# Kernel optimization log

Hardware: AMD Instinct MI355X
Metric: run time of the kernel (lower is better)

Reference implementation:

```python
import jax, jax.numpy as jnp
import numpy as np

N_NODES = 50000
N_EDGES = 800000
IN_DIM = 128
HID = 8
HEADS = 8
OUT_DIM = 64
NEG_SLOPE = 0.2


def setup_inputs() -> dict:
    key = jax.random.key(0)
    ks = jax.random.split(key, 8)
    x = jax.random.normal(ks[0], (N_NODES, IN_DIM), dtype=jnp.float32)
    edge_index = jax.random.randint(ks[1], (2, N_EDGES), 0, N_NODES, dtype=jnp.int64)
    W1 = jax.random.normal(ks[2], (IN_DIM, HEADS * HID), dtype=jnp.float32) / np.sqrt(IN_DIM)
    a_src1 = jax.random.normal(ks[3], (HEADS, HID), dtype=jnp.float32)
    a_dst1 = jax.random.normal(ks[4], (HEADS, HID), dtype=jnp.float32)
    b1 = jnp.zeros((HEADS * HID,), dtype=jnp.float32)
    W2 = jax.random.normal(ks[5], (HEADS * HID, OUT_DIM), dtype=jnp.float32) / np.sqrt(HEADS * HID)
    a_src2 = jax.random.normal(ks[6], (1, OUT_DIM), dtype=jnp.float32)
    a_dst2 = jax.random.normal(ks[7], (1, OUT_DIM), dtype=jnp.float32)
    b2 = jnp.zeros((OUT_DIM,), dtype=jnp.float32)
    return {"x": x, "edge_index": edge_index, "W1": W1, "a_src1": a_src1,
            "a_dst1": a_dst1, "b1": b1, "W2": W2, "a_src2": a_src2,
            "a_dst2": a_dst2, "b2": b2}


def gat_conv(x, src, dst, W, a_src, a_dst, b, heads, ch):
    # PyG GATConv (eval mode): linear -> per-edge LeakyReLU score ->
    # segment-softmax over incoming edges -> weighted scatter-add -> +bias
    n = x.shape[0]
    h = (x @ W).reshape(n, heads, ch)               # [N,H,C]
    score_src = jnp.einsum('nhc,hc->nh', h, a_src)  # [N,H]
    score_dst = jnp.einsum('nhc,hc->nh', h, a_dst)  # [N,H]
    e = jax.nn.leaky_relu(score_src[src] + score_dst[dst], NEG_SLOPE)  # [E,H]
    m = jax.ops.segment_max(e, dst, num_segments=n)
    m = jnp.where(jnp.isfinite(m), m, 0.0)
    p = jnp.exp(e - m[dst])
    denom = jax.ops.segment_sum(p, dst, num_segments=n)
    alpha = p / (denom[dst] + 1e-16)                # [E,H]
    out = jax.ops.segment_sum(h[src] * alpha[:, :, None], dst, num_segments=n)
    return out.reshape(n, heads * ch) + b


def reference(x, edge_index, W1, a_src1, a_dst1, b1, W2, a_src2, a_dst2, b2):
    n = x.shape[0]
    # add_self_loops=True (PyG default)
    loops = jnp.arange(n, dtype=edge_index.dtype)
    src = jnp.concatenate([edge_index[0], loops])
    dst = jnp.concatenate([edge_index[1], loops])
    h = gat_conv(x, src, dst, W1, a_src1, a_dst1, b1, HEADS, HID)
    h = jax.nn.elu(h)
    out = gat_conv(h, src, dst, W2, a_src2, a_dst2, b2, 1, OUT_DIM)
    return out
```

## Files before the change

kernel.cpp:

```cpp
#include <hip/hip_runtime.h>
#include <hip/hip_fp16.h>
#include <math.h>
#include <stdint.h>

#define N_NODES 50000
#define N_EDGES 800000
#define ET (N_EDGES + N_NODES)
#define IN_DIM 128
#define H1DIM 64
#define HEADS 8
#define HID 8
#define OUT_DIM 64
#define NEG_SLOPE 0.2f

#define SCAN_TILE 256
#define NTILES ((N_NODES + SCAN_TILE - 1) / SCAN_TILE)
#define RC 8
#define PF 6

#define LIN1_WAVES (N_NODES / 16)
#define LIN1_BLOCKS ((LIN1_WAVES + 3) / 4)
#define LIN2_WAVES (N_NODES / 16)
#define LIN2_BLOCKS ((LIN2_WAVES + 3) / 4)
#define EB ((ET + 255) / 256)

typedef _Float16 half8 __attribute__((ext_vector_type(8)));
typedef float f32x4 __attribute__((ext_vector_type(4)));

__device__ __forceinline__ float lrelu(float v) { return v >= 0.f ? v : NEG_SLOPE * v; }

__device__ __forceinline__ int xcc_id() {
    int v;
    asm volatile("s_getreg_b32 %0, hwreg(HW_REG_XCC_ID)" : "=s"(v));
    return v & 7;
}

__device__ __forceinline__ void fma8raw(uint4 u, float alpha, float* a) {
    float2 f0 = __half22float2(*(const __half2*)&u.x);
    float2 f1 = __half22float2(*(const __half2*)&u.y);
    float2 f2 = __half22float2(*(const __half2*)&u.z);
    float2 f3 = __half22float2(*(const __half2*)&u.w);
    a[0] += f0.x * alpha; a[1] += f0.y * alpha;
    a[2] += f1.x * alpha; a[3] += f1.y * alpha;
    a[4] += f2.x * alpha; a[5] += f2.y * alpha;
    a[6] += f3.x * alpha; a[7] += f3.y * alpha;
}

__device__ __forceinline__ void fma8h(const __half* __restrict__ base, float alpha, float* a) {
    fma8raw(*reinterpret_cast<const uint4*>(base), alpha, a);
}

__device__ __forceinline__ void edge_nodes(const int* __restrict__ ei, int e, int& s, int& d) {
    if (e < N_EDGES) { s = ei[e]; d = ei[N_EDGES + e]; }
    else             { s = e - N_EDGES; d = s; }
}


__global__ __launch_bounds__(256) void cl1_kernel(
    const int* __restrict__ ei, int* __restrict__ cnt8, int* __restrict__ pos,
    const float* __restrict__ x, const float* __restrict__ W1,
    const float* __restrict__ a_src, const float* __restrict__ a_dst,
    __half* __restrict__ h1, float* __restrict__ ssrc, float* __restrict__ sdst)
{
    if (blockIdx.x >= LIN1_BLOCKS) {
        int i = (blockIdx.x - LIN1_BLOCKS) * 256 + threadIdx.x;
        if (i >= ET) return;
        int s, d; edge_nodes(ei, i, s, d);
        int c = xcc_id();
        int r = atomicAdd(&cnt8[c * N_NODES + d], 1);
        pos[i] = r | (c << 28);
        return;
    }

    __shared__ __half bH[16 * 512];
    __shared__ __half bL[16 * 512];

    int tid = threadIdx.x;
    #pragma unroll
    for (int i = 0; i < 32; ++i) {
        int idx = i * 256 + tid;
        int f = idx >> 9, rr = idx & 511;
        int l = rr >> 3, j = rr & 7;
        int ks = f >> 2, ct = f & 3;
        int k = ks * 32 + ((l >> 4) << 3) + j;
        int c = (ct << 4) + (l & 15);
        float w = W1[k * 64 + c];
        __half hi = __float2half(w);
        bH[idx] = hi;
        bL[idx] = __float2half(w - __half2float(hi));
    }
    __syncthreads();

    int wid = tid >> 6, t = tid & 63;
    int g = blockIdx.x * 4 + wid;
    if (g >= LIN1_WAVES) return;
    int n0 = g * 16;
    int row = t & 15, kq = t >> 4;

    f32x4 acc[4] = {};
    const float* xp = x + (size_t)(n0 + row) * IN_DIM + kq * 8;
    #pragma unroll
    for (int ks = 0; ks < 4; ++ks) {
        float4 u0 = *reinterpret_cast<const float4*>(xp + ks * 32);
        float4 u1 = *reinterpret_cast<const float4*>(xp + ks * 32 + 4);
        float xv[8] = {u0.x, u0.y, u0.z, u0.w, u1.x, u1.y, u1.z, u1.w};
        half8 ah, al;
        #pragma unroll
        for (int j = 0; j < 8; ++j) {
            _Float16 h = (_Float16)xv[j];
            ah[j] = h;
            al[j] = (_Float16)(xv[j] - (float)h);
        }
        #pragma unroll
        for (int ct = 0; ct < 4; ++ct) {
            int f = ks * 4 + ct;
            half8 bh = *reinterpret_cast<const half8*>(&bH[f * 512 + t * 8]);
            half8 bl = *reinterpret_cast<const half8*>(&bL[f * 512 + t * 8]);
            acc[ct] = __builtin_amdgcn_mfma_f32_16x16x32_f16(ah, bh, acc[ct], 0, 0, 0);
            acc[ct] = __builtin_amdgcn_mfma_f32_16x16x32_f16(al, bh, acc[ct], 0, 0, 0);
            acc[ct] = __builtin_amdgcn_mfma_f32_16x16x32_f16(ah, bl, acc[ct], 0, 0, 0);
        }
    }

    float asv[4], adv[4];
    #pragma unroll
    for (int ct = 0; ct < 4; ++ct) {
        asv[ct] = a_src[ct * 16 + (t & 15)];
        adv[ct] = a_dst[ct * 16 + (t & 15)];
    }
    int rbase = n0 + (t >> 4) * 4;
    #pragma unroll
    for (int r = 0; r < 4; ++r) {
        int n = rbase + r;
        #pragma unroll
        for (int ct = 0; ct < 4; ++ct) {
            float v = acc[ct][r];
            h1[(size_t)n * 64 + ct * 16 + (t & 15)] = __float2half(v);
            float ps = v * asv[ct], pd = v * adv[ct];
            ps += __shfl_xor(ps, 1); ps += __shfl_xor(ps, 2); ps += __shfl_xor(ps, 4);
            pd += __shfl_xor(pd, 1); pd += __shfl_xor(pd, 2); pd += __shfl_xor(pd, 4);
            if ((t & 7) == 0) {
                int hd = ct * 2 + ((t >> 3) & 1);
                ssrc[n * 8 + hd] = ps;
                sdst[n * 8 + hd] = pd;
            }
        }
    }
}


__global__ __launch_bounds__(SCAN_TILE) void scanA_kernel(
    const int* __restrict__ cnt8, int* __restrict__ row, int* __restrict__ aux)
{
    __shared__ int sh[SCAN_TILE];
    int t = threadIdx.x, i = blockIdx.x * SCAN_TILE + t;
    int v = 0;
    if (i < N_NODES) {
        #pragma unroll
        for (int c = 0; c < 8; ++c) v += cnt8[c * N_NODES + i];
    }
    sh[t] = v;
    __syncthreads();
    #pragma unroll
    for (int off = 1; off < SCAN_TILE; off <<= 1) {
        int add = (t >= off) ? sh[t - off] : 0;
        __syncthreads();
        sh[t] += add;
        __syncthreads();
    }
    if (i < N_NODES) row[i] = sh[t] - v;
    if (t == SCAN_TILE - 1) aux[blockIdx.x] = sh[t];
}

__global__ __launch_bounds__(SCAN_TILE) void scanB_kernel(int* __restrict__ aux, int* __restrict__ row) {
    __shared__ int sh[SCAN_TILE];
    int t = threadIdx.x;
    int v = (t < NTILES) ? aux[t] : 0;
    sh[t] = v;
    __syncthreads();
    #pragma unroll
    for (int off = 1; off < SCAN_TILE; off <<= 1) {
        int add = (t >= off) ? sh[t - off] : 0;
        __syncthreads();
        sh[t] += add;
        __syncthreads();
    }
    if (t < NTILES) aux[t] = sh[t] - v;
    if (t == NTILES - 1) row[N_NODES] = sh[t];
}

__global__ __launch_bounds__(SCAN_TILE) void scanC_kernel(
    const int* __restrict__ aux, int* __restrict__ row,
    const int* __restrict__ cnt8, int* __restrict__ off8)
{
    int i = blockIdx.x * SCAN_TILE + threadIdx.x;
    if (i >= N_NODES) return;
    int r = row[i] + aux[i >> 8];
    row[i] = r;
    int run = r;
    #pragma unroll
    for (int c = 0; c < 8; ++c) {
        off8[c * N_NODES + i] = run;
        run += cnt8[c * N_NODES + i];
    }
}

__global__ void fill_kernel(const int* __restrict__ ei, const int* __restrict__ off8,
                            const int* __restrict__ pos, int* __restrict__ adj)
{
    int i = blockIdx.x * blockDim.x + threadIdx.x;
    if (i >= ET) return;
    int s, d; edge_nodes(ei, i, s, d);
    int pr = pos[i];
    int c = (unsigned)pr >> 28;
    int r = pr & 0x0FFFFFFF;
    adj[off8[c * N_NODES + d] + r] = s;
}


__global__ __launch_bounds__(256) void l1_kernel(
    const int* __restrict__ row, const int* __restrict__ adj,
    const __half* __restrict__ h1, const float* __restrict__ s1, const float* __restrict__ t1,
    const float* __restrict__ b1, float* __restrict__ ha)
{
    int wid = threadIdx.x >> 6, t = threadIdx.x & 63;
    int half = t >> 5, tt = t & 31;
    int n = blockIdx.x * 8 + wid * 2 + half;
    int beg = row[n], end = row[n + 1];
    int slot = tt >> 3, h = tt & 7;
    float sd = t1[n * 8 + h];
    const int e0 = beg + slot;

    int   sv[RC];
    float p[RC];
    uint4 raw[PF];
    float m = -3e38f;
    #pragma unroll
    for (int it = 0; it < RC; ++it) {
        int e = e0 + it * 4;
        bool ok = e < end;
        int s = ok ? adj[e] : n;
        sv[it] = s;
        float v = ok ? lrelu(s1[s * 8 + h] + sd) : -3e38f;
        p[it] = v;
        m = fmaxf(m, v);
        if (it < PF) raw[it] = *reinterpret_cast<const uint4*>(h1 + (size_t)s * 64 + h * 8);
    }
    for (int e = e0 + RC * 4; e < end; e += 4)
        m = fmaxf(m, lrelu(s1[adj[e] * 8 + h] + sd));
    m = fmaxf(m, __shfl_xor(m, 8));
    m = fmaxf(m, __shfl_xor(m, 16));

    float den = 0.f;
    #pragma unroll
    for (int it = 0; it < RC; ++it) {
        float pe = __expf(p[it] - m);
        p[it] = pe;
        den += pe;
    }
    for (int e = e0 + RC * 4; e < end; e += 4)
        den += __expf(lrelu(s1[adj[e] * 8 + h] + sd) - m);
    den += __shfl_xor(den, 8);
    den += __shfl_xor(den, 16);
    float inv = 1.f / (den + 1e-16f);

    float a[8] = {0,0,0,0,0,0,0,0};
    #pragma unroll
    for (int it = 0; it < PF; ++it) fma8raw(raw[it], p[it] * inv, a);
    #pragma unroll
    for (int it = PF; it < RC; ++it) {
        int e = e0 + it * 4;
        if (e < end) fma8h(h1 + (size_t)sv[it] * 64 + h * 8, p[it] * inv, a);
    }
    for (int e = e0 + RC * 4; e < end; e += 4) {
        int s = adj[e];
        float alpha = __expf(lrelu(s1[s * 8 + h] + sd) - m) * inv;
        fma8h(h1 + (size_t)s * 64 + h * 8, alpha, a);
    }
    #pragma unroll
    for (int j = 0; j < 8; ++j) {
        a[j] += __shfl_xor(a[j], 8);
        a[j] += __shfl_xor(a[j], 16);
    }

    int j0 = slot * 2;
    float v0 = a[j0]     + b1[h * 8 + j0];
    float v1 = a[j0 + 1] + b1[h * 8 + j0 + 1];
    v0 = v0 > 0.f ? v0 : (__expf(v0) - 1.f);
    v1 = v1 > 0.f ? v1 : (__expf(v1) - 1.f);
    *reinterpret_cast<float2*>(ha + (size_t)n * 64 + h * 8 + j0) = make_float2(v0, v1);
}


__global__ __launch_bounds__(256) void lin2_kernel(
    const float* __restrict__ ha, const float* __restrict__ W2,
    const float* __restrict__ as2, const float* __restrict__ ad2,
    __half* __restrict__ h2, float* __restrict__ s2, float* __restrict__ t2)
{
    __shared__ __half bH[8 * 512];
    __shared__ __half bL[8 * 512];

    int tid = threadIdx.x;
    #pragma unroll
    for (int i = 0; i < 16; ++i) {
        int idx = i * 256 + tid;
        int f = idx >> 9, rr = idx & 511;
        int l = rr >> 3, j = rr & 7;
        int ks = f >> 2, ct = f & 3;
        int k = ks * 32 + ((l >> 4) << 3) + j;
        int c = (ct << 4) + (l & 15);
        float w = W2[k * 64 + c];
        __half hi = __float2half(w);
        bH[idx] = hi;
        bL[idx] = __float2half(w - __half2float(hi));
    }
    __syncthreads();

    int wid = tid >> 6, t = tid & 63;
    int g = blockIdx.x * 4 + wid;
    if (g >= LIN2_WAVES) return;
    int n0 = g * 16;
    int row = t & 15, kq = t >> 4;

    f32x4 acc[4] = {};
    const float* xp = ha + (size_t)(n0 + row) * 64 + kq * 8;
    #pragma unroll
    for (int ks = 0; ks < 2; ++ks) {
        float4 u0 = *reinterpret_cast<const float4*>(xp + ks * 32);
        float4 u1 = *reinterpret_cast<const float4*>(xp + ks * 32 + 4);
        float xv[8] = {u0.x, u0.y, u0.z, u0.w, u1.x, u1.y, u1.z, u1.w};
        half8 ah, al;
        #pragma unroll
        for (int j = 0; j < 8; ++j) {
            _Float16 hh = (_Float16)xv[j];
            ah[j] = hh;
            al[j] = (_Float16)(xv[j] - (float)hh);
        }
        #pragma unroll
        for (int ct = 0; ct < 4; ++ct) {
            int f = ks * 4 + ct;
            half8 bh = *reinterpret_cast<const half8*>(&bH[f * 512 + t * 8]);
            half8 bl = *reinterpret_cast<const half8*>(&bL[f * 512 + t * 8]);
            acc[ct] = __builtin_amdgcn_mfma_f32_16x16x32_f16(ah, bh, acc[ct], 0, 0, 0);
            acc[ct] = __builtin_amdgcn_mfma_f32_16x16x32_f16(al, bh, acc[ct], 0, 0, 0);
            acc[ct] = __builtin_amdgcn_mfma_f32_16x16x32_f16(ah, bl, acc[ct], 0, 0, 0);
        }
    }

    float asv[4], adv[4];
    #pragma unroll
    for (int ct = 0; ct < 4; ++ct) {
        asv[ct] = as2[ct * 16 + (t & 15)];
        adv[ct] = ad2[ct * 16 + (t & 15)];
    }
    int rbase = n0 + (t >> 4) * 4;
    #pragma unroll
    for (int r = 0; r < 4; ++r) {
        int n = rbase + r;
        float ps = 0.f, pd = 0.f;
        #pragma unroll
        for (int ct = 0; ct < 4; ++ct) {
            float v = acc[ct][r];
            h2[(size_t)n * 64 + ct * 16 + (t & 15)] = __float2half(v);
            ps += v * asv[ct];
            pd += v * adv[ct];
        }
        ps += __shfl_xor(ps, 1); ps += __shfl_xor(ps, 2);
        ps += __shfl_xor(ps, 4); ps += __shfl_xor(ps, 8);
        pd += __shfl_xor(pd, 1); pd += __shfl_xor(pd, 2);
        pd += __shfl_xor(pd, 4); pd += __shfl_xor(pd, 8);
        if ((t & 15) == 0) { s2[n] = ps; t2[n] = pd; }
    }
}


__global__ __launch_bounds__(256) void l2_kernel(
    const int* __restrict__ row, const int* __restrict__ adj,
    const __half* __restrict__ h2, const float* __restrict__ s2, const float* __restrict__ t2,
    const float* __restrict__ b2, float* __restrict__ out)
{
    int wid = threadIdx.x >> 6, t = threadIdx.x & 63;
    int half = t >> 5, tt = t & 31;
    int n = blockIdx.x * 8 + wid * 2 + half;
    int beg = row[n], end = row[n + 1];
    int slot = tt >> 3, g = tt & 7;
    float sd = t2[n];
    const int e0 = beg + slot;

    int   sv[RC];
    float p[RC];
    uint4 raw[PF];
    float m = -3e38f;
    #pragma unroll
    for (int it = 0; it < RC; ++it) {
        int e = e0 + it * 4;
        bool ok = e < end;
        int s = ok ? adj[e] : n;
        sv[it] = s;
        float v = ok ? lrelu(s2[s] + sd) : -3e38f;
        p[it] = v;
        m = fmaxf(m, v);
        if (it < PF) raw[it] = *reinterpret_cast<const uint4*>(h2 + (size_t)s * 64 + g * 8);
    }
    for (int e = e0 + RC * 4; e < end; e += 4)
        m = fmaxf(m, lrelu(s2[adj[e]] + sd));
    m = fmaxf(m, __shfl_xor(m, 8));
    m = fmaxf(m, __shfl_xor(m, 16));

    float den = 0.f;
    #pragma unroll
    for (int it = 0; it < RC; ++it) {
        float pe = __expf(p[it] - m);
        p[it] = pe;
        den += pe;
    }
    for (int e = e0 + RC * 4; e < end; e += 4)
        den += __expf(lrelu(s2[adj[e]] + sd) - m);
    den += __shfl_xor(den, 8);
    den += __shfl_xor(den, 16);
    float inv = 1.f / (den + 1e-16f);

    float a[8] = {0,0,0,0,0,0,0,0};
    #pragma unroll
    for (int it = 0; it < PF; ++it) fma8raw(raw[it], p[it] * inv, a);
    #pragma unroll
    for (int it = PF; it < RC; ++it) {
        int e = e0 + it * 4;
        if (e < end) fma8h(h2 + (size_t)sv[it] * 64 + g * 8, p[it] * inv, a);
    }
    for (int e = e0 + RC * 4; e < end; e += 4) {
        int s = adj[e];
        float alpha = __expf(lrelu(s2[s] + sd) - m) * inv;
        fma8h(h2 + (size_t)s * 64 + g * 8, alpha, a);
    }
    #pragma unroll
    for (int j = 0; j < 8; ++j) {
        a[j] += __shfl_xor(a[j], 8);
        a[j] += __shfl_xor(a[j], 16);
    }
    if (slot == 0) {
        float4 o0 = make_float4(a[0] + b2[g * 8 + 0], a[1] + b2[g * 8 + 1],
                                a[2] + b2[g * 8 + 2], a[3] + b2[g * 8 + 3]);
        float4 o1 = make_float4(a[4] + b2[g * 8 + 4], a[5] + b2[g * 8 + 5],
                                a[6] + b2[g * 8 + 6], a[7] + b2[g * 8 + 7]);
        float4* op = (float4*)(out + (size_t)n * 64 + g * 8);
        op[0] = o0; op[1] = o1;
    }
}

extern "C" void kernel_launch(void* const* d_in, const int* in_sizes, int n_in,
                              void* d_out, int out_size, void* d_ws, size_t ws_size,
                              hipStream_t stream)
{
    const float* x   = (const float*)d_in[0];
    const int* ei    = (const int*)d_in[1];
    const float* W1  = (const float*)d_in[2];
    const float* as1 = (const float*)d_in[3];
    const float* ad1 = (const float*)d_in[4];
    const float* b1  = (const float*)d_in[5];
    const float* W2  = (const float*)d_in[6];
    const float* as2 = (const float*)d_in[7];
    const float* ad2 = (const float*)d_in[8];
    const float* b2  = (const float*)d_in[9];
    float* out = (float*)d_out;

    char* wsb = (char*)d_ws;
    __half* h1  = (__half*)wsb;
    __half* h2  = h1 + (size_t)N_NODES * 64;
    float*  s1  = (float*)(h2 + (size_t)N_NODES * 64);
    float*  t1  = s1 + N_NODES * 8;
    float*  s2  = t1 + N_NODES * 8;
    float*  t2  = s2 + N_NODES;
    int*    cnt8 = (int*)(t2 + N_NODES);
    int*    off8 = cnt8 + 8 * N_NODES;
    int*    rowp = off8 + 8 * N_NODES;
    int*    aux  = rowp + N_NODES + 1;
    int*    adj  = aux + NTILES;
    int*    pos  = adj + ET;
    float*  ha   = (float*)(((uintptr_t)(pos + ET) + 15) & ~(uintptr_t)15);

    hipMemsetAsync(cnt8, 0, 8 * N_NODES * sizeof(int), stream);

    cl1_kernel<<<LIN1_BLOCKS + EB, 256, 0, stream>>>(ei, cnt8, pos, x, W1, as1, ad1, h1, s1, t1);

    scanA_kernel<<<NTILES, SCAN_TILE, 0, stream>>>(cnt8, rowp, aux);
    scanB_kernel<<<1, SCAN_TILE, 0, stream>>>(aux, rowp);
    scanC_kernel<<<NTILES, SCAN_TILE, 0, stream>>>(aux, rowp, cnt8, off8);
    fill_kernel<<<EB, 256, 0, stream>>>(ei, off8, pos, adj);

    l1_kernel<<<N_NODES / 8, 256, 0, stream>>>(rowp, adj, h1, s1, t1, b1, ha);

    lin2_kernel<<<LIN2_BLOCKS, 256, 0, stream>>>(ha, W2, as2, ad2, h2, s2, t2);

    l2_kernel<<<N_NODES / 8, 256, 0, stream>>>(rowp, adj, h2, s2, t2, b2, out);
}
```

Before: 215.2 us.

## Precompute split-fp16 weights, store ELU output in fp16, handle self-loops in scan

Adds a prep kernel that converts W1 and W2 once into hi/lo fp16 fragment layouts and zeroes the counters, replacing the memset and the per-block shared-memory weight conversion in cl1 and lin2. Self-loops no longer go through the edge counting and fill path; the scan adds one to each node's count and scanC writes the self index at the end of each row. Edge counting and fill now handle four edges per thread. The layer-1 ELU output is stored as fp16, so lin2 loads half8 directly and drops the low-part MFMA for activations, which reduces precision in layer 2.

```diff
diff --git a/kernel.cpp b/kernel.cpp
--- a/kernel.cpp
+++ b/kernel.cpp
@@ -22,7 +22,11 @@
 #define LIN1_BLOCKS ((LIN1_WAVES + 3) / 4)
 #define LIN2_WAVES (N_NODES / 16)
 #define LIN2_BLOCKS ((LIN2_WAVES + 3) / 4)
-#define EB ((ET + 255) / 256)
+
+#define EPT 4
+#define CB ((N_EDGES + 256*EPT - 1) / (256*EPT))
+#define FB CB
+#define ZB ((8 * N_NODES + 255) / 256)
 
 typedef _Float16 half8 __attribute__((ext_vector_type(8)));
 typedef float f32x4 __attribute__((ext_vector_type(4)));
@@ -50,35 +54,16 @@
     fma8raw(*reinterpret_cast<const uint4*>(base), alpha, a);
 }
 
-__device__ __forceinline__ void edge_nodes(const int* __restrict__ ei, int e, int& s, int& d) {
-    if (e < N_EDGES) { s = ei[e]; d = ei[N_EDGES + e]; }
-    else             { s = e - N_EDGES; d = s; }
-}
-
-
-__global__ __launch_bounds__(256) void cl1_kernel(
-    const int* __restrict__ ei, int* __restrict__ cnt8, int* __restrict__ pos,
-    const float* __restrict__ x, const float* __restrict__ W1,
-    const float* __restrict__ a_src, const float* __restrict__ a_dst,
-    __half* __restrict__ h1, float* __restrict__ ssrc, float* __restrict__ sdst)
-{
-    if (blockIdx.x >= LIN1_BLOCKS) {
-        int i = (blockIdx.x - LIN1_BLOCKS) * 256 + threadIdx.x;
-        if (i >= ET) return;
-        int s, d; edge_nodes(ei, i, s, d);
-        int c = xcc_id();
-        int r = atomicAdd(&cnt8[c * N_NODES + d], 1);
-        pos[i] = r | (c << 28);
-        return;
-    }
-
-    __shared__ __half bH[16 * 512];
-    __shared__ __half bL[16 * 512];
-
-    int tid = threadIdx.x;
-    #pragma unroll
-    for (int i = 0; i < 32; ++i) {
-        int idx = i * 256 + tid;
+
+__global__ __launch_bounds__(256) void prep_kernel(
+    const float* __restrict__ W1, const float* __restrict__ W2,
+    __half* __restrict__ w1fH, __half* __restrict__ w1fL,
+    __half* __restrict__ w2fH, __half* __restrict__ w2fL,
+    int* __restrict__ cnt8)
+{
+    int b = blockIdx.x;
+    if (b < 32) {
+        int idx = b * 256 + threadIdx.x;
         int f = idx >> 9, rr = idx & 511;
         int l = rr >> 3, j = rr & 7;
         int ks = f >> 2, ct = f & 3;
@@ -86,13 +71,50 @@
         int c = (ct << 4) + (l & 15);
         float w = W1[k * 64 + c];
         __half hi = __float2half(w);
-        bH[idx] = hi;
-        bL[idx] = __float2half(w - __half2float(hi));
-    }
-    __syncthreads();
-
-    int wid = tid >> 6, t = tid & 63;
-    int g = blockIdx.x * 4 + wid;
+        w1fH[idx] = hi;
+        w1fL[idx] = __float2half(w - __half2float(hi));
+    } else if (b < 48) {
+        int idx = (b - 32) * 256 + threadIdx.x;
+        int f = idx >> 9, rr = idx & 511;
+        int l = rr >> 3, j = rr & 7;
+        int ks = f >> 2, ct = f & 3;
+        int k = ks * 32 + ((l >> 4) << 3) + j;
+        int c = (ct << 4) + (l & 15);
+        float w = W2[k * 64 + c];
+        __half hi = __float2half(w);
+        w2fH[idx] = hi;
+        w2fL[idx] = __float2half(w - __half2float(hi));
+    } else {
+        int i = (b - 48) * 256 + threadIdx.x;
+        if (i < 8 * N_NODES) cnt8[i] = 0;
+    }
+}
+
+
+__global__ __launch_bounds__(256) void cl1_kernel(
+    const int* __restrict__ ei, int* __restrict__ cnt8, int* __restrict__ pos,
+    const float* __restrict__ x,
+    const __half* __restrict__ w1fH, const __half* __restrict__ w1fL,
+    const float* __restrict__ a_src, const float* __restrict__ a_dst,
+    __half* __restrict__ h1, float* __restrict__ ssrc, float* __restrict__ sdst)
+{
+    if (blockIdx.x < CB) {
+        int base = blockIdx.x * (256 * EPT) + threadIdx.x;
+        int c = xcc_id();
+        #pragma unroll
+        for (int j = 0; j < EPT; ++j) {
+            int e = base + j * 256;
+            if (e < N_EDGES) {
+                int d = ei[N_EDGES + e];
+                int r = atomicAdd(&cnt8[c * N_NODES + d], 1);
+                pos[e] = r | (c << 28);
+            }
+        }
+        return;
+    }
+
+    int wid = threadIdx.x >> 6, t = threadIdx.x & 63;
+    int g = (blockIdx.x - CB) * 4 + wid;
     if (g >= LIN1_WAVES) return;
     int n0 = g * 16;
     int row = t & 15, kq = t >> 4;
@@ -114,8 +136,8 @@
         #pragma unroll
         for (int ct = 0; ct < 4; ++ct) {
             int f = ks * 4 + ct;
-            half8 bh = *reinterpret_cast<const half8*>(&bH[f * 512 + t * 8]);
-            half8 bl = *reinterpret_cast<const half8*>(&bL[f * 512 + t * 8]);
+            half8 bh = *reinterpret_cast<const half8*>(w1fH + f * 512 + t * 8);
+            half8 bl = *reinterpret_cast<const half8*>(w1fL + f * 512 + t * 8);
             acc[ct] = __builtin_amdgcn_mfma_f32_16x16x32_f16(ah, bh, acc[ct], 0, 0, 0);
             acc[ct] = __builtin_amdgcn_mfma_f32_16x16x32_f16(al, bh, acc[ct], 0, 0, 0);
             acc[ct] = __builtin_amdgcn_mfma_f32_16x16x32_f16(ah, bl, acc[ct], 0, 0, 0);
@@ -156,6 +178,7 @@
     int t = threadIdx.x, i = blockIdx.x * SCAN_TILE + t;
     int v = 0;
     if (i < N_NODES) {
+        v = 1;
         #pragma unroll
         for (int c = 0; c < 8; ++c) v += cnt8[c * N_NODES + i];
     }
@@ -191,7 +214,7 @@
 
 __global__ __launch_bounds__(SCAN_TILE) void scanC_kernel(
     const int* __restrict__ aux, int* __restrict__ row,
-    const int* __restrict__ cnt8, int* __restrict__ off8)
+    const int* __restrict__ cnt8, int* __restrict__ off8, int* __restrict__ adj)
 {
     int i = blockIdx.x * SCAN_TILE + threadIdx.x;
     if (i >= N_NODES) return;
@@ -203,25 +226,32 @@
         off8[c * N_NODES + i] = run;
         run += cnt8[c * N_NODES + i];
     }
-}
-
-__global__ void fill_kernel(const int* __restrict__ ei, const int* __restrict__ off8,
-                            const int* __restrict__ pos, int* __restrict__ adj)
-{
-    int i = blockIdx.x * blockDim.x + threadIdx.x;
-    if (i >= ET) return;
-    int s, d; edge_nodes(ei, i, s, d);
-    int pr = pos[i];
-    int c = (unsigned)pr >> 28;
-    int r = pr & 0x0FFFFFFF;
-    adj[off8[c * N_NODES + d] + r] = s;
+    adj[run] = i;
+}
+
+__global__ __launch_bounds__(256) void fill_kernel(
+    const int* __restrict__ ei, const int* __restrict__ off8,
+    const int* __restrict__ pos, int* __restrict__ adj)
+{
+    int base = blockIdx.x * (256 * EPT) + threadIdx.x;
+    #pragma unroll
+    for (int j = 0; j < EPT; ++j) {
+        int e = base + j * 256;
+        if (e < N_EDGES) {
+            int s = ei[e], d = ei[N_EDGES + e];
+            int pr = pos[e];
+            int c = (unsigned)pr >> 28;
+            int r = pr & 0x0FFFFFFF;
+            adj[off8[c * N_NODES + d] + r] = s;
+        }
+    }
 }
 
 
 __global__ __launch_bounds__(256) void l1_kernel(
     const int* __restrict__ row, const int* __restrict__ adj,
     const __half* __restrict__ h1, const float* __restrict__ s1, const float* __restrict__ t1,
-    const float* __restrict__ b1, float* __restrict__ ha)
+    const float* __restrict__ b1, __half* __restrict__ ha)
 {
     int wid = threadIdx.x >> 6, t = threadIdx.x & 63;
     int half = t >> 5, tt = t & 31;
@@ -288,34 +318,20 @@
     float v1 = a[j0 + 1] + b1[h * 8 + j0 + 1];
     v0 = v0 > 0.f ? v0 : (__expf(v0) - 1.f);
     v1 = v1 > 0.f ? v1 : (__expf(v1) - 1.f);
-    *reinterpret_cast<float2*>(ha + (size_t)n * 64 + h * 8 + j0) = make_float2(v0, v1);
+    __half2 hv;
+    hv.x = __float2half(v0);
+    hv.y = __float2half(v1);
+    *reinterpret_cast<__half2*>(ha + (size_t)n * 64 + h * 8 + j0) = hv;
 }
 
 
 __global__ __launch_bounds__(256) void lin2_kernel(
-    const float* __restrict__ ha, const float* __restrict__ W2,
+    const __half* __restrict__ ha,
+    const __half* __restrict__ w2fH, const __half* __restrict__ w2fL,
     const float* __restrict__ as2, const float* __restrict__ ad2,
     __half* __restrict__ h2, float* __restrict__ s2, float* __restrict__ t2)
 {
-    __shared__ __half bH[8 * 512];
-    __shared__ __half bL[8 * 512];
-
     int tid = threadIdx.x;
-    #pragma unroll
-    for (int i = 0; i < 16; ++i) {
-        int idx = i * 256 + tid;
-        int f = idx >> 9, rr = idx & 511;
-        int l = rr >> 3, j = rr & 7;
-        int ks = f >> 2, ct = f & 3;
-        int k = ks * 32 + ((l >> 4) << 3) + j;
-        int c = (ct << 4) + (l & 15);
-        float w = W2[k * 64 + c];
-        __half hi = __float2half(w);
-        bH[idx] = hi;
-        bL[idx] = __float2half(w - __half2float(hi));
-    }
-    __syncthreads();
-
     int wid = tid >> 6, t = tid & 63;
     int g = blockIdx.x * 4 + wid;
     if (g >= LIN2_WAVES) return;
@@ -323,27 +339,17 @@
     int row = t & 15, kq = t >> 4;
 
     f32x4 acc[4] = {};
-    const float* xp = ha + (size_t)(n0 + row) * 64 + kq * 8;
+    const __half* xp = ha + (size_t)(n0 + row) * 64 + kq * 8;
     #pragma unroll
     for (int ks = 0; ks < 2; ++ks) {
-        float4 u0 = *reinterpret_cast<const float4*>(xp + ks * 32);
-        float4 u1 = *reinterpret_cast<const float4*>(xp + ks * 32 + 4);
-        float xv[8] = {u0.x, u0.y, u0.z, u0.w, u1.x, u1.y, u1.z, u1.w};
-        half8 ah, al;
-        #pragma unroll
-        for (int j = 0; j < 8; ++j) {
-            _Float16 hh = (_Float16)xv[j];
-            ah[j] = hh;
-            al[j] = (_Float16)(xv[j] - (float)hh);
-        }
+        half8 ahv = *reinterpret_cast<const half8*>(xp + ks * 32);
         #pragma unroll
         for (int ct = 0; ct < 4; ++ct) {
             int f = ks * 4 + ct;
-            half8 bh = *reinterpret_cast<const half8*>(&bH[f * 512 + t * 8]);
-            half8 bl = *reinterpret_cast<const half8*>(&bL[f * 512 + t * 8]);
-            acc[ct] = __builtin_amdgcn_mfma_f32_16x16x32_f16(ah, bh, acc[ct], 0, 0, 0);
-            acc[ct] = __builtin_amdgcn_mfma_f32_16x16x32_f16(al, bh, acc[ct], 0, 0, 0);
-            acc[ct] = __builtin_amdgcn_mfma_f32_16x16x32_f16(ah, bl, acc[ct], 0, 0, 0);
+            half8 bh = *reinterpret_cast<const half8*>(w2fH + f * 512 + t * 8);
+            half8 bl = *reinterpret_cast<const half8*>(w2fL + f * 512 + t * 8);
+            acc[ct] = __builtin_amdgcn_mfma_f32_16x16x32_f16(ahv, bh, acc[ct], 0, 0, 0);
+            acc[ct] = __builtin_amdgcn_mfma_f32_16x16x32_f16(ahv, bl, acc[ct], 0, 0, 0);
         }
     }
 
@@ -465,32 +471,37 @@
     float* out = (float*)d_out;
 
     char* wsb = (char*)d_ws;
-    __half* h1  = (__half*)wsb;
-    __half* h2  = h1 + (size_t)N_NODES * 64;
-    float*  s1  = (float*)(h2 + (size_t)N_NODES * 64);
-    float*  t1  = s1 + N_NODES * 8;
-    float*  s2  = t1 + N_NODES * 8;
-    float*  t2  = s2 + N_NODES;
+    __half* h1   = (__half*)wsb;
+    __half* h2   = h1 + (size_t)N_NODES * 64;
+    __half* ha   = h2 + (size_t)N_NODES * 64;
+    __half* w1fH = ha + (size_t)N_NODES * 64;
+    __half* w1fL = w1fH + 8192;
+    __half* w2fH = w1fL + 8192;
+    __half* w2fL = w2fH + 4096;
+    float*  s1   = (float*)(w2fL + 4096);
+    float*  t1   = s1 + N_NODES * 8;
+    float*  s2   = t1 + N_NODES * 8;
+    float*  t2   = s2 + N_NODES;
     int*    cnt8 = (int*)(t2 + N_NODES);
     int*    off8 = cnt8 + 8 * N_NODES;
     int*    rowp = off8 + 8 * N_NODES;
     int*    aux  = rowp + N_NODES + 1;
     int*    adj  = aux + NTILES;
     int*    pos  = adj + ET;
-    float*  ha   = (float*)(((uintptr_t)(pos + ET) + 15) & ~(uintptr_t)15);
-
-    hipMemsetAsync(cnt8, 0, 8 * N_NODES * sizeof(int), stream);
-
-    cl1_kernel<<<LIN1_BLOCKS + EB, 256, 0, stream>>>(ei, cnt8, pos, x, W1, as1, ad1, h1, s1, t1);
+
+    prep_kernel<<<48 + ZB, 256, 0, stream>>>(W1, W2, w1fH, w1fL, w2fH, w2fL, cnt8);
+
+    cl1_kernel<<<CB + LIN1_BLOCKS, 256, 0, stream>>>(ei, cnt8, pos, x, w1fH, w1fL,
+                                                     as1, ad1, h1, s1, t1);
 
     scanA_kernel<<<NTILES, SCAN_TILE, 0, stream>>>(cnt8, rowp, aux);
     scanB_kernel<<<1, SCAN_TILE, 0, stream>>>(aux, rowp);
-    scanC_kernel<<<NTILES, SCAN_TILE, 0, stream>>>(aux, rowp, cnt8, off8);
-    fill_kernel<<<EB, 256, 0, stream>>>(ei, off8, pos, adj);
+    scanC_kernel<<<NTILES, SCAN_TILE, 0, stream>>>(aux, rowp, cnt8, off8, adj);
+    fill_kernel<<<FB, 256, 0, stream>>>(ei, off8, pos, adj);
 
     l1_kernel<<<N_NODES / 8, 256, 0, stream>>>(rowp, adj, h1, s1, t1, b1, ha);
 
-    lin2_kernel<<<LIN2_BLOCKS, 256, 0, stream>>>(ha, W2, as2, ad2, h2, s2, t2);
+    lin2_kernel<<<LIN2_BLOCKS, 256, 0, stream>>>(ha, w2fH, w2fL, as2, ad2, h2, s2, t2);
 
     l2_kernel<<<N_NODES / 8, 256, 0, stream>>>(rowp, adj, h2, s2, t2, b2, out);
 }
```

After: 218.1 us. Within noise of the previous version (+1.4%).
